# Performance work log

Hardware: AMD Instinct MI355X
Metric: run time of the kernel (lower is better)

Reference implementation:

```python
import jax, jax.numpy as jnp
import numpy as np

N = 50000          # nodes (spots/cells)
E = 1000000        # edges, avg degree 20
IN_DIM, HID, OUT = 256, 128, 64
R = 2              # num_relations
NEG_SLOPE = 0.2    # PyG RGATConv default


def setup_inputs() -> dict:
    key = jax.random.key(0)
    ks = jax.random.split(key, 12)
    features = jax.random.normal(ks[0], (N, IN_DIM), jnp.float32)
    edge_index = jax.random.randint(ks[1], (2, E), 0, N)
    edge_type = jax.random.randint(ks[2], (E,), 0, R)
    s_in, s_hid, s_out = 1.0 / np.sqrt(IN_DIM), 1.0 / np.sqrt(HID), 1.0 / np.sqrt(OUT)
    # RGATConv layer 1 (heads=1, dim=1): relation weights + shared q,k
    W1 = jax.random.normal(ks[3], (R, IN_DIM, HID), jnp.float32) * s_in
    q1 = jax.random.normal(ks[4], (HID, 1), jnp.float32) * s_hid
    k1 = jax.random.normal(ks[5], (HID, 1), jnp.float32) * s_hid
    # RGATConv layer 2
    W2 = jax.random.normal(ks[6], (R, HID, OUT), jnp.float32) * s_hid
    q2 = jax.random.normal(ks[7], (OUT, 1), jnp.float32) * s_out
    k2 = jax.random.normal(ks[8], (OUT, 1), jnp.float32) * s_out
    # decoder: Linear(OUT->HID) then Linear(HID->IN_DIM), biases default-on
    dec_w1 = jax.random.normal(ks[9], (HID, OUT), jnp.float32) * s_out
    dec_b1 = jnp.zeros((HID,), jnp.float32)
    dec_w2 = jax.random.normal(ks[10], (IN_DIM, HID), jnp.float32) * s_hid
    dec_b2 = jnp.zeros((IN_DIM,), jnp.float32)
    return dict(features=features, edge_index=edge_index, edge_type=edge_type,
                W1=W1, q1=q1, k1=k1, W2=W2, q2=q2, k2=k2,
                dec_w1=dec_w1, dec_b1=dec_b1, dec_w2=dec_w2, dec_b2=dec_b2)


def _segment_softmax(alpha, index, num_segments):
    # softmax over edges grouped by destination node (PyG softmax, +1e-16 denom)
    amax = jax.ops.segment_max(alpha, index, num_segments=num_segments)
    amax = jnp.where(jnp.isfinite(amax), amax, 0.0)  # empty segments -> -inf
    ex = jnp.exp(alpha - amax[index])
    denom = jax.ops.segment_sum(ex, index, num_segments=num_segments)
    return ex / (denom[index] + 1e-16)


def _rgat_layer(x, W, q, k, src, dst, edge_type, num_nodes):
    # per-edge x_e @ W[edge_type[e]] == project all nodes per relation, then gather
    proj = jnp.einsum('ni,rio->rno', x, W)          # (R, N, O)
    out_i = proj[edge_type, dst]                    # (E, O) dest-node projection
    out_j = proj[edge_type, src]                    # (E, O) src-node projection
    alpha = jax.nn.leaky_relu(out_i @ q + out_j @ k, NEG_SLOPE)  # (E, 1)
    alpha = _segment_softmax(alpha, dst, num_nodes)
    out = jax.ops.segment_sum(alpha * out_j, dst, num_segments=num_nodes)  # (N, O)
    return out, alpha


def reference(features, edge_index, edge_type, W1, q1, k1, W2, q2, k2,
              dec_w1, dec_b1, dec_w2, dec_b2):
    src, dst = edge_index[0], edge_index[1]
    n = features.shape[0]
    h1, att1 = _rgat_layer(features, W1, q1, k1, src, dst, edge_type, n)
    h1 = jax.nn.elu(h1)
    h2, att2 = _rgat_layer(h1, W2, q2, k2, src, dst, edge_type, n)
    h2 = jax.nn.elu(h2)
    h3 = (h2 @ dec_w1.T + dec_b1) @ dec_w2.T + dec_b2
    return h2, h3, att1, att2
```

## Files before the change

### kernel.cpp

```cpp
#include <hip/hip_runtime.h>
#include <hip/hip_bf16.h>

static constexpr int N_NODES = 50000;
static constexpr int N_EDGE  = 1000000;
static constexpr int IN_D    = 256;
static constexpr int HID_D   = 128;
static constexpr int OUT_D   = 64;
static constexpr int R_REL   = 2;

typedef __attribute__((ext_vector_type(8))) short short8;
typedef __attribute__((ext_vector_type(8))) unsigned short ushort8;
typedef __attribute__((ext_vector_type(4))) float float4v;

static __device__ __forceinline__ unsigned short f2bf(float v) {
    __hip_bfloat16 h = __float2bfloat16(v);
    return *(unsigned short*)&h;
}
static __device__ __forceinline__ float bf2f(unsigned short u) {
    union { unsigned int i; float f; } c; c.i = ((unsigned int)u) << 16; return c.f;
}
static __device__ __forceinline__ float bflo(unsigned u) {
    union { unsigned i; float f; } c; c.i = u << 16; return c.f;
}
static __device__ __forceinline__ float bfhi(unsigned u) {
    union { unsigned i; float f; } c; c.i = u & 0xFFFF0000u; return c.f;
}
static __device__ __forceinline__ float u2f(unsigned u) {
    union { unsigned i; float f; } c; c.i = u; return c.f;
}
static __device__ __forceinline__ unsigned f2u(float f) {
    union { unsigned i; float f; } c; c.f = f; return c.i;
}
static __device__ __forceinline__ void acc8(float w, uint4 v, float (&a)[8]) {
    a[0] = fmaf(w, bflo(v.x), a[0]); a[1] = fmaf(w, bfhi(v.x), a[1]);
    a[2] = fmaf(w, bflo(v.y), a[2]); a[3] = fmaf(w, bfhi(v.y), a[3]);
    a[4] = fmaf(w, bflo(v.z), a[4]); a[5] = fmaf(w, bfhi(v.z), a[5]);
    a[6] = fmaf(w, bflo(v.w), a[6]); a[7] = fmaf(w, bfhi(v.w), a[7]);
}

__global__ __launch_bounds__(256) void prep_k(
    const float* __restrict__ W1, const float* __restrict__ W2,
    const float* __restrict__ dw1, const float* __restrict__ dw2,
    unsigned short* __restrict__ Wc1t, unsigned short* __restrict__ Wc2t,
    unsigned short* __restrict__ dw1h, unsigned short* __restrict__ dw1l,
    unsigned short* __restrict__ dw2h, unsigned short* __restrict__ dw2l)
{
    int idx = blockIdx.x * 256 + threadIdx.x;
    if (idx < R_REL * HID_D * IN_D) {
        const int n = idx / IN_D, kk = idx % IN_D;
        const int r = n / HID_D, o = n % HID_D;
        Wc1t[(long)n * IN_D + kk] = f2bf(W1[((long)r * IN_D + kk) * HID_D + o]);
        return;
    }
    idx -= R_REL * HID_D * IN_D;
    if (idx < R_REL * OUT_D * HID_D) {
        const int n = idx / HID_D, kk = idx % HID_D;
        const int r = n / OUT_D, o = n % OUT_D;
        Wc2t[(long)n * HID_D + kk] = f2bf(W2[((long)r * HID_D + kk) * OUT_D + o]);
        return;
    }
    idx -= R_REL * OUT_D * HID_D;
    if (idx < HID_D * OUT_D) {
        const float v = dw1[idx];
        const unsigned short hi = f2bf(v);
        dw1h[idx] = hi; dw1l[idx] = f2bf(v - bf2f(hi));
        return;
    }
    idx -= HID_D * OUT_D;
    if (idx < IN_D * HID_D) {
        const float v = dw2[idx];
        const unsigned short hi = f2bf(v);
        dw2h[idx] = hi; dw2l[idx] = f2bf(v - bf2f(hi));
    }
}

template<int TM, bool CVT>
__global__ __launch_bounds__(256) void gemm_bf16_k(
    const unsigned short* __restrict__ A, const float* __restrict__ Af,
    const unsigned short* __restrict__ Bt,
    unsigned short* __restrict__ Cb, int M, int K, int Nn)
{
    constexpr int BM = TM * 32;
    constexpr int LDK = 40;
    __shared__ __align__(16) unsigned short As[BM * LDK];
    __shared__ __align__(16) unsigned short Bs[128 * LDK];

    const int tid = threadIdx.x;
    const int wave = tid >> 6, lane = tid & 63;
    const int wm = (wave >> 1) * (TM * 16);
    const int wn = (wave & 1) * 64;
    const int bm = blockIdx.y * BM;
    const int bn = blockIdx.x * 128;
    const int l15 = lane & 15, quad = lane >> 4;

    float4v acc[TM][4];
#pragma unroll
    for (int i = 0; i < TM; ++i)
#pragma unroll
        for (int j = 0; j < 4; ++j) acc[i][j] = (float4v){0.f, 0.f, 0.f, 0.f};

    for (int k0 = 0; k0 < K; k0 += 32) {
        for (int c = tid; c < BM * 4; c += 256) {
            const int r = c >> 2, ch = c & 3;
            const int gr = min(bm + r, M - 1);
            if constexpr (CVT) {
                const float4 f0 = *(const float4*)&Af[(long)gr * K + k0 + ch * 8];
                const float4 f1 = *(const float4*)&Af[(long)gr * K + k0 + ch * 8 + 4];
                uint4 o;
                o.x = (unsigned)f2bf(f0.x) | ((unsigned)f2bf(f0.y) << 16);
                o.y = (unsigned)f2bf(f0.z) | ((unsigned)f2bf(f0.w) << 16);
                o.z = (unsigned)f2bf(f1.x) | ((unsigned)f2bf(f1.y) << 16);
                o.w = (unsigned)f2bf(f1.z) | ((unsigned)f2bf(f1.w) << 16);
                *(uint4*)&As[r * LDK + ch * 8] = o;
            } else {
                *(uint4*)&As[r * LDK + ch * 8] =
                    *(const uint4*)&A[(long)gr * K + k0 + ch * 8];
            }
        }
        for (int c = tid; c < 128 * 4; c += 256) {
            const int r = c >> 2, ch = c & 3;
            *(uint4*)&Bs[r * LDK + ch * 8] =
                *(const uint4*)&Bt[(long)(bn + r) * K + k0 + ch * 8];
        }
        __syncthreads();

        short8 bfrag[4];
#pragma unroll
        for (int nt = 0; nt < 4; ++nt)
            bfrag[nt] = *(const short8*)&Bs[(wn + nt * 16 + l15) * LDK + quad * 8];
#pragma unroll
        for (int mt = 0; mt < TM; ++mt) {
            const short8 afrag = *(const short8*)&As[(wm + mt * 16 + l15) * LDK + quad * 8];
#pragma unroll
            for (int nt = 0; nt < 4; ++nt)
                acc[mt][nt] = __builtin_amdgcn_mfma_f32_16x16x32_bf16(
                    afrag, bfrag[nt], acc[mt][nt], 0, 0, 0);
        }
        __syncthreads();
    }

#pragma unroll
    for (int mt = 0; mt < TM; ++mt)
#pragma unroll
        for (int nt = 0; nt < 4; ++nt) {
            const int n = bn + wn + nt * 16 + l15;
#pragma unroll
            for (int rg = 0; rg < 4; ++rg) {
                const int m = bm + wm + mt * 16 + quad * 4 + rg;
                if (m < M) Cb[(long)m * Nn + n] = f2bf(acc[mt][nt][rg]);
            }
        }
}

template<int TM, bool SPLITOUT>
__global__ __launch_bounds__(256) void dec_gemm_k(
    const unsigned short* __restrict__ Ah, const unsigned short* __restrict__ Al,
    const unsigned short* __restrict__ Bh, const unsigned short* __restrict__ Bl,
    const float* __restrict__ bias, float* __restrict__ Cf,
    unsigned short* __restrict__ Ch, unsigned short* __restrict__ Cl,
    int M, int K, int Nn)
{
    constexpr int BM = TM * 32;
    constexpr int LDK = 40;
    __shared__ __align__(16) unsigned short Ash[BM * LDK];
    __shared__ __align__(16) unsigned short Asl[BM * LDK];
    __shared__ __align__(16) unsigned short Bsh[128 * LDK];
    __shared__ __align__(16) unsigned short Bsl[128 * LDK];

    const int tid = threadIdx.x;
    const int wave = tid >> 6, lane = tid & 63;
    const int wm = (wave >> 1) * (TM * 16);
    const int wn = (wave & 1) * 64;
    const int bm = blockIdx.y * BM;
    const int bn = blockIdx.x * 128;
    const int l15 = lane & 15, quad = lane >> 4;

    float4v acc[TM][4];
#pragma unroll
    for (int i = 0; i < TM; ++i)
#pragma unroll
        for (int j = 0; j < 4; ++j) acc[i][j] = (float4v){0.f, 0.f, 0.f, 0.f};

    for (int k0 = 0; k0 < K; k0 += 32) {
        for (int c = tid; c < BM * 4; c += 256) {
            const int r = c >> 2, ch = c & 3;
            const int gr = min(bm + r, M - 1);
            *(uint4*)&Ash[r * LDK + ch * 8] =
                *(const uint4*)&Ah[(long)gr * K + k0 + ch * 8];
            *(uint4*)&Asl[r * LDK + ch * 8] =
                *(const uint4*)&Al[(long)gr * K + k0 + ch * 8];
        }
        for (int c = tid; c < 128 * 4; c += 256) {
            const int r = c >> 2, ch = c & 3;
            *(uint4*)&Bsh[r * LDK + ch * 8] =
                *(const uint4*)&Bh[(long)(bn + r) * K + k0 + ch * 8];
            *(uint4*)&Bsl[r * LDK + ch * 8] =
                *(const uint4*)&Bl[(long)(bn + r) * K + k0 + ch * 8];
        }
        __syncthreads();

        short8 bh[4], bl[4];
#pragma unroll
        for (int nt = 0; nt < 4; ++nt) {
            bh[nt] = *(const short8*)&Bsh[(wn + nt * 16 + l15) * LDK + quad * 8];
            bl[nt] = *(const short8*)&Bsl[(wn + nt * 16 + l15) * LDK + quad * 8];
        }
#pragma unroll
        for (int mt = 0; mt < TM; ++mt) {
            const short8 ah = *(const short8*)&Ash[(wm + mt * 16 + l15) * LDK + quad * 8];
            const short8 al = *(const short8*)&Asl[(wm + mt * 16 + l15) * LDK + quad * 8];
#pragma unroll
            for (int nt = 0; nt < 4; ++nt) {
                acc[mt][nt] = __builtin_amdgcn_mfma_f32_16x16x32_bf16(ah, bh[nt], acc[mt][nt], 0, 0, 0);
                acc[mt][nt] = __builtin_amdgcn_mfma_f32_16x16x32_bf16(al, bh[nt], acc[mt][nt], 0, 0, 0);
                acc[mt][nt] = __builtin_amdgcn_mfma_f32_16x16x32_bf16(ah, bl[nt], acc[mt][nt], 0, 0, 0);
            }
        }
        __syncthreads();
    }

#pragma unroll
    for (int mt = 0; mt < TM; ++mt)
#pragma unroll
        for (int nt = 0; nt < 4; ++nt) {
            const int n = bn + wn + nt * 16 + l15;
            const float bv = bias[n];
#pragma unroll
            for (int rg = 0; rg < 4; ++rg) {
                const int m = bm + wm + mt * 16 + quad * 4 + rg;
                if (m >= M) continue;
                const float v = acc[mt][nt][rg] + bv;
                if (SPLITOUT) {
                    const unsigned short hi = f2bf(v);
                    Ch[(long)m * Nn + n] = hi;
                    Cl[(long)m * Nn + n] = f2bf(v - bf2f(hi));
                } else {
                    Cf[(long)m * Nn + n] = v;
                }
            }
        }
}

template<int D>
__global__ __launch_bounds__(256) void dotsB_k(
    const unsigned short* __restrict__ projb, const float* __restrict__ q,
    const float* __restrict__ k, float* __restrict__ qd, float* __restrict__ kd,
    int Nn)
{
    const int node = (int)((blockIdx.x * (long)blockDim.x + threadIdx.x) >> 6);
    const int lane = threadIdx.x & 63;
    if (node >= Nn) return;
    const unsigned short* row = projb + (long)node * (2 * D);
    float sq0, sk0, sq1, sk1;
    if (D == 128) {
        const ushort2 a = *(const ushort2*)(row + 2 * lane);
        const ushort2 b = *(const ushort2*)(row + 128 + 2 * lane);
        const float q0 = q[2 * lane], q1 = q[2 * lane + 1];
        const float c0 = k[2 * lane], c1 = k[2 * lane + 1];
        const float a0 = bf2f(a.x), a1 = bf2f(a.y);
        const float b0 = bf2f(b.x), b1 = bf2f(b.y);
        sq0 = fmaf(a0, q0, a1 * q1); sk0 = fmaf(a0, c0, a1 * c1);
        sq1 = fmaf(b0, q0, b1 * q1); sk1 = fmaf(b0, c0, b1 * c1);
    } else {
        const float a0 = bf2f(row[lane]), b0 = bf2f(row[64 + lane]);
        const float q0 = q[lane], c0 = k[lane];
        sq0 = a0 * q0; sk0 = a0 * c0;
        sq1 = b0 * q0; sk1 = b0 * c0;
    }
#pragma unroll
    for (int off = 32; off; off >>= 1) {
        sq0 += __shfl_xor(sq0, off); sk0 += __shfl_xor(sk0, off);
        sq1 += __shfl_xor(sq1, off); sk1 += __shfl_xor(sk1, off);
    }
    if (lane == 0) {
        *(float2*)&qd[2 * node] = make_float2(sq0, sq1);
        kd[node] = sk0; kd[Nn + node] = sk1;
    }
}

__global__ __launch_bounds__(256) void rank_k(
    const int* __restrict__ dstv, int* __restrict__ cnt,
    int* __restrict__ rank, int E)
{
    const int e = blockIdx.x * blockDim.x + threadIdx.x;
    if (e >= E) return;
    rank[e] = atomicAdd(&cnt[dstv[e]], 1);
}

__global__ __launch_bounds__(256) void scan1_k(
    const int* __restrict__ cnt, int* __restrict__ excl_out,
    int* __restrict__ bsum, int n)
{
    __shared__ int s[256];
    const int t = threadIdx.x;
    const int i = blockIdx.x * 256 + t;
    const int v = (i < n) ? cnt[i] : 0;
    s[t] = v;
    __syncthreads();
    for (int off = 1; off < 256; off <<= 1) {
        const int x = (t >= off) ? s[t - off] : 0;
        __syncthreads();
        s[t] += x;
        __syncthreads();
    }
    if (i < n) excl_out[i] = s[t] - v;
    if (t == 255) bsum[blockIdx.x] = s[255];
}

__global__ __launch_bounds__(256) void scan2_k(
    int* __restrict__ bsum, int* __restrict__ bpre, int nb)
{
    __shared__ int s[256];
    const int t = threadIdx.x;
    const int v = (t < nb) ? bsum[t] : 0;
    s[t] = v;
    __syncthreads();
    for (int off = 1; off < 256; off <<= 1) {
        const int x = (t >= off) ? s[t - off] : 0;
        __syncthreads();
        s[t] += x;
        __syncthreads();
    }
    if (t < nb) bpre[t] = s[t] - v;
}

__global__ __launch_bounds__(256) void scan3_k(
    int* __restrict__ excl, const int* __restrict__ bpre,
    int* __restrict__ offs, int n, int total)
{
    const int i = blockIdx.x * 256 + threadIdx.x;
    if (i >= n) return;
    offs[i] = excl[i] + bpre[i >> 8];
    if (i == 0) offs[n] = total;
}

__global__ __launch_bounds__(256) void place_k(
    const int* __restrict__ srcv, const int* __restrict__ dstv,
    const int* __restrict__ et, const int* __restrict__ rank,
    const int* __restrict__ offs, unsigned* __restrict__ recs, int E)
{
    const int e = blockIdx.x * blockDim.x + threadIdx.x;
    if (e >= E) return;
    const int pos = offs[dstv[e]] + rank[e];
    recs[pos] = (unsigned)((et[e] << 16) | srcv[e]);
}

__global__ __launch_bounds__(256) void aggr1_k(
    const int* __restrict__ offs, const unsigned* __restrict__ recs,
    const float* __restrict__ qd, const float* __restrict__ kd,
    const unsigned short* __restrict__ projb,
    float* __restrict__ inv_out, unsigned short* __restrict__ h1b, int Nn)
{
    __shared__ uint2 sh[4][64];
    const int wid = threadIdx.x >> 6;
    const int d = blockIdx.x * 4 + wid;
    const int lane = threadIdx.x & 63;
    if (d >= Nn) return;
    const int beg = offs[d], end = offs[d + 1];
    const float2 qv = *(const float2*)&qd[2 * d];
    const char* pb = (const char*)projb;
    const int quarter = lane >> 4, l15 = lane & 15;
    const unsigned lb = (unsigned)(l15 << 4);
    uint2* shl = sh[wid];

    float exsum = 0.f;
    float a[8] = {0.f, 0.f, 0.f, 0.f, 0.f, 0.f, 0.f, 0.f};

    for (int b = beg; b < end; b += 64) {
        const int i = b + lane;
        float ex = 0.f; unsigned off = 0;
        if (i < end) {
            const unsigned rx = recs[i];
            const int s = (int)(rx & 0xFFFFu), t = (int)(rx >> 16);
            float av = (t ? qv.y : qv.x) + kd[t * Nn + s];
            av = av > 0.f ? av : 0.2f * av;
            ex = __expf(av);
            off = ((unsigned)s << 9) | ((unsigned)t << 8);
        }
        shl[lane] = make_uint2(f2u(ex), off);
        exsum += ex;

        const int cnt = min(64, end - b);
        for (int j = 0; j < cnt; j += 16) {
            const uint2 p0 = shl[j + quarter];
            const uint2 p1 = shl[j + 4 + quarter];
            const uint2 p2 = shl[j + 8 + quarter];
            const uint2 p3 = shl[j + 12 + quarter];
            const uint4 v0 = *(const uint4*)(pb + (p0.y + lb));
            const uint4 v1 = *(const uint4*)(pb + (p1.y + lb));
            const uint4 v2 = *(const uint4*)(pb + (p2.y + lb));
            const uint4 v3 = *(const uint4*)(pb + (p3.y + lb));
            acc8(u2f(p0.x), v0, a);
            acc8(u2f(p1.x), v1, a);
            acc8(u2f(p2.x), v2, a);
            acc8(u2f(p3.x), v3, a);
        }
    }
#pragma unroll
    for (int o = 32; o; o >>= 1) exsum += __shfl_xor(exsum, o);
    const float inv = 1.f / (exsum + 1e-16f);
    if (lane == 0) inv_out[d] = inv;
#pragma unroll
    for (int q = 0; q < 8; ++q) {
        a[q] += __shfl_xor(a[q], 32);
        a[q] += __shfl_xor(a[q], 16);
    }
    if (quarter == 0) {
        ushort8 st;
#pragma unroll
        for (int q = 0; q < 8; ++q) {
            const float e = a[q] * inv;
            st[q] = f2bf(e > 0.f ? e : expm1f(e));
        }
        *(ushort8*)&h1b[(long)d * 128 + (l15 << 3)] = st;
    }
}

__global__ __launch_bounds__(256) void aggr2_k(
    const int* __restrict__ offs, const unsigned* __restrict__ recs,
    const float* __restrict__ qd, const float* __restrict__ kd,
    const unsigned short* __restrict__ projb,
    float* __restrict__ inv_out, float* __restrict__ out,
    unsigned short* __restrict__ h2h, unsigned short* __restrict__ h2l, int Nn)
{
    __shared__ uint2 sh[4][64];
    const int wid = threadIdx.x >> 6;
    const int d = blockIdx.x * 4 + wid;
    const int lane = threadIdx.x & 63;
    if (d >= Nn) return;
    const int beg = offs[d], end = offs[d + 1];
    const float2 qv = *(const float2*)&qd[2 * d];
    const char* pb = (const char*)projb;
    const int eighth = lane >> 3, l7 = lane & 7;
    const unsigned lb = (unsigned)(l7 << 4);
    uint2* shl = sh[wid];

    float exsum = 0.f;
    float a[8] = {0.f, 0.f, 0.f, 0.f, 0.f, 0.f, 0.f, 0.f};

    for (int b = beg; b < end; b += 64) {
        const int i = b + lane;
        float ex = 0.f; unsigned off = 0;
        if (i < end) {
            const unsigned rx = recs[i];
            const int s = (int)(rx & 0xFFFFu), t = (int)(rx >> 16);
            float av = (t ? qv.y : qv.x) + kd[t * Nn + s];
            av = av > 0.f ? av : 0.2f * av;
            ex = __expf(av);
            off = ((unsigned)s << 8) | ((unsigned)t << 7);
        }
        shl[lane] = make_uint2(f2u(ex), off);
        exsum += ex;

        const int cnt = min(64, end - b);
        for (int j = 0; j < cnt; j += 32) {
            const uint2 p0 = shl[j + eighth];
            const uint2 p1 = shl[j + 8 + eighth];
            const uint2 p2 = shl[j + 16 + eighth];
            const uint2 p3 = shl[j + 24 + eighth];
            const uint4 v0 = *(const uint4*)(pb + (p0.y + lb));
            const uint4 v1 = *(const uint4*)(pb + (p1.y + lb));
            const uint4 v2 = *(const uint4*)(pb + (p2.y + lb));
            const uint4 v3 = *(const uint4*)(pb + (p3.y + lb));
            acc8(u2f(p0.x), v0, a);
            acc8(u2f(p1.x), v1, a);
            acc8(u2f(p2.x), v2, a);
            acc8(u2f(p3.x), v3, a);
        }
    }
#pragma unroll
    for (int o = 32; o; o >>= 1) exsum += __shfl_xor(exsum, o);
    const float inv = 1.f / (exsum + 1e-16f);
    if (lane == 0) inv_out[d] = inv;
#pragma unroll
    for (int q = 0; q < 8; ++q) {
        a[q] += __shfl_xor(a[q], 32);
        a[q] += __shfl_xor(a[q], 16);
        a[q] += __shfl_xor(a[q], 8);
    }
    if (eighth == 0) {
        float vv[8];
#pragma unroll
        for (int q = 0; q < 8; ++q) {
            const float e = a[q] * inv;
            vv[q] = e > 0.f ? e : expm1f(e);
        }
        float4 f0; f0.x = vv[0]; f0.y = vv[1]; f0.z = vv[2]; f0.w = vv[3];
        float4 f1; f1.x = vv[4]; f1.y = vv[5]; f1.z = vv[6]; f1.w = vv[7];
        *(float4*)&out[(long)d * 64 + (l7 << 3)] = f0;
        *(float4*)&out[(long)d * 64 + (l7 << 3) + 4] = f1;
        ushort8 hh, hl;
#pragma unroll
        for (int q = 0; q < 8; ++q) {
            const unsigned short hi = f2bf(vv[q]);
            hh[q] = hi; hl[q] = f2bf(vv[q] - bf2f(hi));
        }
        *(ushort8*)&h2h[(long)d * 64 + (l7 << 3)] = hh;
        *(ushort8*)&h2l[(long)d * 64 + (l7 << 3)] = hl;
    }
}

__global__ __launch_bounds__(256) void att_k(
    const int* __restrict__ srcv, const int* __restrict__ dstv,
    const int* __restrict__ et,
    const float* __restrict__ qd1, const float* __restrict__ kd1,
    const float* __restrict__ inv1,
    const float* __restrict__ qd2, const float* __restrict__ kd2,
    const float* __restrict__ inv2,
    float* __restrict__ att1, float* __restrict__ att2, int E, int Nn)
{
    const int e = blockIdx.x * 256 + threadIdx.x;
    if (e >= E) return;
    const int s = srcv[e], d = dstv[e], t = et[e];
    float x1 = qd1[2 * d + t] + kd1[t * Nn + s];
    x1 = x1 > 0.f ? x1 : 0.2f * x1;
    att1[e] = __expf(x1) * inv1[d];
    float x2 = qd2[2 * d + t] + kd2[t * Nn + s];
    x2 = x2 > 0.f ? x2 : 0.2f * x2;
    att2[e] = __expf(x2) * inv2[d];
}

extern "C" void kernel_launch(void* const* d_in, const int* in_sizes, int n_in,
                              void* d_out, int out_size, void* d_ws, size_t ws_size,
                              hipStream_t stream)
{
    const float* features = (const float*)d_in[0];
    const int*   eidx     = (const int*)d_in[1];
    const int*   etype    = (const int*)d_in[2];
    const float* W1       = (const float*)d_in[3];
    const float* q1       = (const float*)d_in[4];
    const float* k1       = (const float*)d_in[5];
    const float* W2       = (const float*)d_in[6];
    const float* q2       = (const float*)d_in[7];
    const float* k2       = (const float*)d_in[8];
    const float* dw1      = (const float*)d_in[9];
    const float* db1      = (const float*)d_in[10];
    const float* dw2      = (const float*)d_in[11];
    const float* db2      = (const float*)d_in[12];

    const int* srcv = eidx;
    const int* dstv = eidx + N_EDGE;

    float* out_h2 = (float*)d_out;
    float* out_h3 = out_h2 + (long)N_NODES * OUT_D;
    float* att1   = out_h3 + (long)N_NODES * IN_D;
    float* att2   = att1 + N_EDGE;

    char* W = (char*)d_ws;
    int* rank = (int*)W;
    unsigned short* projb1 = (unsigned short*)(W);
    unsigned short* projb2 = (unsigned short*)(W);
    unsigned short* hidh   = (unsigned short*)(W);
    unsigned short* hidl   = (unsigned short*)(W + 12800000);
    unsigned short* h1b    = (unsigned short*)(W + 25600000);
    unsigned short* h2h    = (unsigned short*)(W + 25600000 + 12800000);
    unsigned short* h2l    = (unsigned short*)(W + 25600000 + 19200000);
    float* qd1 = (float*)(W + 51200000);
    float* kd1 = qd1 + 2 * N_NODES;
    float* qd2 = kd1 + 2 * N_NODES;
    float* kd2 = qd2 + 2 * N_NODES;
    int* cnt    = (int*)(kd2 + 2 * N_NODES);
    int* offs   = cnt + N_NODES;
    int* bsum   = offs + N_NODES + 1;
    int* bpre   = bsum + 256;
    int* excl   = bpre + 256;
    float* inv1 = (float*)(W + 53500000);
    float* inv2 = inv1 + N_NODES;
    unsigned* recs = (unsigned*)(W + 57300000);
    unsigned short* Wc1t = (unsigned short*)(W + 65300000);
    unsigned short* Wc2t = Wc1t + 65536;
    unsigned short* dw1h = Wc2t + 16384;
    unsigned short* dw1l = dw1h + 8192;
    unsigned short* dw2h = dw1l + 8192;
    unsigned short* dw2l = dw2h + 32768;

    const int NB = (N_NODES + 255) / 256;

    prep_k<<<480, 256, 0, stream>>>(W1, W2, dw1, dw2,
                                    Wc1t, Wc2t, dw1h, dw1l, dw2h, dw2l);

    hipMemsetAsync(cnt, 0, sizeof(int) * N_NODES, stream);
    rank_k<<<(N_EDGE + 255) / 256, 256, 0, stream>>>(dstv, cnt, rank, N_EDGE);
    scan1_k<<<NB, 256, 0, stream>>>(cnt, excl, bsum, N_NODES);
    scan2_k<<<1, 256, 0, stream>>>(bsum, bpre, NB);
    scan3_k<<<NB, 256, 0, stream>>>(excl, bpre, offs, N_NODES, N_EDGE);
    place_k<<<(N_EDGE + 255) / 256, 256, 0, stream>>>(
        srcv, dstv, etype, rank, offs, recs, N_EDGE);

    gemm_bf16_k<4, true><<<dim3(2, (N_NODES + 127) / 128), 256, 0, stream>>>(
        nullptr, features, Wc1t, projb1, N_NODES, IN_D, 2 * HID_D);
    dotsB_k<128><<<(int)(((long)N_NODES * 64 + 255) / 256), 256, 0, stream>>>(
        projb1, q1, k1, qd1, kd1, N_NODES);
    aggr1_k<<<(N_NODES + 3) / 4, 256, 0, stream>>>(
        offs, recs, qd1, kd1, projb1, inv1, h1b, N_NODES);

    gemm_bf16_k<4, false><<<dim3(1, (N_NODES + 127) / 128), 256, 0, stream>>>(
        h1b, nullptr, Wc2t, projb2, N_NODES, HID_D, 2 * OUT_D);
    dotsB_k<64><<<(int)(((long)N_NODES * 64 + 255) / 256), 256, 0, stream>>>(
        projb2, q2, k2, qd2, kd2, N_NODES);
    aggr2_k<<<(N_NODES + 3) / 4, 256, 0, stream>>>(
        offs, recs, qd2, kd2, projb2, inv2, out_h2, h2h, h2l, N_NODES);

    att_k<<<(N_EDGE + 255) / 256, 256, 0, stream>>>(
        srcv, dstv, etype, qd1, kd1, inv1, qd2, kd2, inv2, att1, att2,
        N_EDGE, N_NODES);

    dec_gemm_k<4, true><<<dim3(1, (N_NODES + 127) / 128), 256, 0, stream>>>(
        h2h, h2l, dw1h, dw1l, db1, nullptr, hidh, hidl, N_NODES, OUT_D, HID_D);
    dec_gemm_k<4, false><<<dim3(2, (N_NODES + 127) / 128), 256, 0, stream>>>(
        hidh, hidl, dw2h, dw2l, db2, out_h3, nullptr, nullptr, N_NODES, HID_D, IN_D);
}
```

Before: 420.8 us.

## Register-prefetch next K-tile in GEMMs and halve M-tile to 64 rows

The bf16 GEMM and split-precision decoder GEMM kernels now load the next K-slice from global memory into registers while MFMAs run on the current LDS tile, then commit it to shared memory after the loop. The goal is to hide global load latency behind compute. All four GEMM launches also move from 128-row to 64-row tiles (TM=2), which doubles the block count for better CU occupancy and load balance. In exchange, register pressure rises and B tiles are reloaded more often.

After: 480.6 us. +14.2%, slower.

```diff
diff --git a/kernel.cpp b/kernel.cpp
--- a/kernel.cpp
+++ b/kernel.cpp
@@ -82,6 +82,8 @@
 {
     constexpr int BM = TM * 32;
     constexpr int LDK = 40;
+    constexpr int ACV = BM / 32;
+    constexpr int ABF = BM / 64;
     __shared__ __align__(16) unsigned short As[BM * LDK];
     __shared__ __align__(16) unsigned short Bs[128 * LDK];
 
@@ -93,36 +95,67 @@
     const int bn = blockIdx.x * 128;
     const int l15 = lane & 15, quad = lane >> 4;
 
+    float4 pa[ACV > 0 ? ACV : 1];
+    uint4  qa[ABF > 0 ? ABF : 1];
+    uint4  qb[2];
+
+    auto prefetch = [&](int k0) {
+        if constexpr (CVT) {
+#pragma unroll
+            for (int i = 0; i < ACV; ++i) {
+                const int q = tid + 256 * i, row = q >> 3, c4 = q & 7;
+                const int gr = min(bm + row, M - 1);
+                pa[i] = *(const float4*)&Af[(long)gr * K + k0 + c4 * 4];
+            }
+        } else {
+#pragma unroll
+            for (int i = 0; i < ABF; ++i) {
+                const int q = tid + 256 * i, row = q >> 2, c8 = q & 3;
+                const int gr = min(bm + row, M - 1);
+                qa[i] = *(const uint4*)&A[(long)gr * K + k0 + c8 * 8];
+            }
+        }
+#pragma unroll
+        for (int i = 0; i < 2; ++i) {
+            const int q = tid + 256 * i, row = q >> 2, c8 = q & 3;
+            qb[i] = *(const uint4*)&Bt[(long)(bn + row) * K + k0 + c8 * 8];
+        }
+    };
+    auto commit = [&]() {
+        if constexpr (CVT) {
+#pragma unroll
+            for (int i = 0; i < ACV; ++i) {
+                const int q = tid + 256 * i, row = q >> 3, c4 = q & 7;
+                uint2 o;
+                o.x = (unsigned)f2bf(pa[i].x) | ((unsigned)f2bf(pa[i].y) << 16);
+                o.y = (unsigned)f2bf(pa[i].z) | ((unsigned)f2bf(pa[i].w) << 16);
+                *(uint2*)&As[row * LDK + c4 * 4] = o;
+            }
+        } else {
+#pragma unroll
+            for (int i = 0; i < ABF; ++i) {
+                const int q = tid + 256 * i, row = q >> 2, c8 = q & 3;
+                *(uint4*)&As[row * LDK + c8 * 8] = qa[i];
+            }
+        }
+#pragma unroll
+        for (int i = 0; i < 2; ++i) {
+            const int q = tid + 256 * i, row = q >> 2, c8 = q & 3;
+            *(uint4*)&Bs[row * LDK + c8 * 8] = qb[i];
+        }
+    };
+
     float4v acc[TM][4];
 #pragma unroll
     for (int i = 0; i < TM; ++i)
 #pragma unroll
         for (int j = 0; j < 4; ++j) acc[i][j] = (float4v){0.f, 0.f, 0.f, 0.f};
 
+    prefetch(0);
     for (int k0 = 0; k0 < K; k0 += 32) {
-        for (int c = tid; c < BM * 4; c += 256) {
-            const int r = c >> 2, ch = c & 3;
-            const int gr = min(bm + r, M - 1);
-            if constexpr (CVT) {
-                const float4 f0 = *(const float4*)&Af[(long)gr * K + k0 + ch * 8];
-                const float4 f1 = *(const float4*)&Af[(long)gr * K + k0 + ch * 8 + 4];
-                uint4 o;
-                o.x = (unsigned)f2bf(f0.x) | ((unsigned)f2bf(f0.y) << 16);
-                o.y = (unsigned)f2bf(f0.z) | ((unsigned)f2bf(f0.w) << 16);
-                o.z = (unsigned)f2bf(f1.x) | ((unsigned)f2bf(f1.y) << 16);
-                o.w = (unsigned)f2bf(f1.z) | ((unsigned)f2bf(f1.w) << 16);
-                *(uint4*)&As[r * LDK + ch * 8] = o;
-            } else {
-                *(uint4*)&As[r * LDK + ch * 8] =
-                    *(const uint4*)&A[(long)gr * K + k0 + ch * 8];
-            }
-        }
-        for (int c = tid; c < 128 * 4; c += 256) {
-            const int r = c >> 2, ch = c & 3;
-            *(uint4*)&Bs[r * LDK + ch * 8] =
-                *(const uint4*)&Bt[(long)(bn + r) * K + k0 + ch * 8];
-        }
-        __syncthreads();
+        commit();
+        __syncthreads();
+        if (k0 + 32 < K) prefetch(k0 + 32);
 
         short8 bfrag[4];
 #pragma unroll
@@ -162,6 +195,7 @@
 {
     constexpr int BM = TM * 32;
     constexpr int LDK = 40;
+    constexpr int ABF = BM / 64;
     __shared__ __align__(16) unsigned short Ash[BM * LDK];
     __shared__ __align__(16) unsigned short Asl[BM * LDK];
     __shared__ __align__(16) unsigned short Bsh[128 * LDK];
@@ -175,29 +209,50 @@
     const int bn = blockIdx.x * 128;
     const int l15 = lane & 15, quad = lane >> 4;
 
+    uint4 pah[ABF > 0 ? ABF : 1], pal[ABF > 0 ? ABF : 1];
+    uint4 pbh[2], pbl[2];
+
+    auto prefetch = [&](int k0) {
+#pragma unroll
+        for (int i = 0; i < ABF; ++i) {
+            const int q = tid + 256 * i, row = q >> 2, c8 = q & 3;
+            const int gr = min(bm + row, M - 1);
+            pah[i] = *(const uint4*)&Ah[(long)gr * K + k0 + c8 * 8];
+            pal[i] = *(const uint4*)&Al[(long)gr * K + k0 + c8 * 8];
+        }
+#pragma unroll
+        for (int i = 0; i < 2; ++i) {
+            const int q = tid + 256 * i, row = q >> 2, c8 = q & 3;
+            pbh[i] = *(const uint4*)&Bh[(long)(bn + row) * K + k0 + c8 * 8];
+            pbl[i] = *(const uint4*)&Bl[(long)(bn + row) * K + k0 + c8 * 8];
+        }
+    };
+    auto commit = [&]() {
+#pragma unroll
+        for (int i = 0; i < ABF; ++i) {
+            const int q = tid + 256 * i, row = q >> 2, c8 = q & 3;
+            *(uint4*)&Ash[row * LDK + c8 * 8] = pah[i];
+            *(uint4*)&Asl[row * LDK + c8 * 8] = pal[i];
+        }
+#pragma unroll
+        for (int i = 0; i < 2; ++i) {
+            const int q = tid + 256 * i, row = q >> 2, c8 = q & 3;
+            *(uint4*)&Bsh[row * LDK + c8 * 8] = pbh[i];
+            *(uint4*)&Bsl[row * LDK + c8 * 8] = pbl[i];
+        }
+    };
+
     float4v acc[TM][4];
 #pragma unroll
     for (int i = 0; i < TM; ++i)
 #pragma unroll
         for (int j = 0; j < 4; ++j) acc[i][j] = (float4v){0.f, 0.f, 0.f, 0.f};
 
+    prefetch(0);
     for (int k0 = 0; k0 < K; k0 += 32) {
-        for (int c = tid; c < BM * 4; c += 256) {
-            const int r = c >> 2, ch = c & 3;
-            const int gr = min(bm + r, M - 1);
-            *(uint4*)&Ash[r * LDK + ch * 8] =
-                *(const uint4*)&Ah[(long)gr * K + k0 + ch * 8];
-            *(uint4*)&Asl[r * LDK + ch * 8] =
-                *(const uint4*)&Al[(long)gr * K + k0 + ch * 8];
-        }
-        for (int c = tid; c < 128 * 4; c += 256) {
-            const int r = c >> 2, ch = c & 3;
-            *(uint4*)&Bsh[r * LDK + ch * 8] =
-                *(const uint4*)&Bh[(long)(bn + r) * K + k0 + ch * 8];
-            *(uint4*)&Bsl[r * LDK + ch * 8] =
-                *(const uint4*)&Bl[(long)(bn + r) * K + k0 + ch * 8];
-        }
-        __syncthreads();
+        commit();
+        __syncthreads();
+        if (k0 + 32 < K) prefetch(k0 + 32);
 
         short8 bh[4], bl[4];
 #pragma unroll
@@ -575,6 +630,7 @@
     unsigned short* dw2l = dw2h + 32768;
 
     const int NB = (N_NODES + 255) / 256;
+    const int MB64 = (N_NODES + 63) / 64;
 
     prep_k<<<480, 256, 0, stream>>>(W1, W2, dw1, dw2,
                                     Wc1t, Wc2t, dw1h, dw1l, dw2h, dw2l);
@@ -587,14 +643,14 @@
     place_k<<<(N_EDGE + 255) / 256, 256, 0, stream>>>(
         srcv, dstv, etype, rank, offs, recs, N_EDGE);
 
-    gemm_bf16_k<4, true><<<dim3(2, (N_NODES + 127) / 128), 256, 0, stream>>>(
+    gemm_bf16_k<2, true><<<dim3(2, MB64), 256, 0, stream>>>(
         nullptr, features, Wc1t, projb1, N_NODES, IN_D, 2 * HID_D);
     dotsB_k<128><<<(int)(((long)N_NODES * 64 + 255) / 256), 256, 0, stream>>>(
         projb1, q1, k1, qd1, kd1, N_NODES);
     aggr1_k<<<(N_NODES + 3) / 4, 256, 0, stream>>>(
         offs, recs, qd1, kd1, projb1, inv1, h1b, N_NODES);
 
-    gemm_bf16_k<4, false><<<dim3(1, (N_NODES + 127) / 128), 256, 0, stream>>>(
+    gemm_bf16_k<2, false><<<dim3(1, MB64), 256, 0, stream>>>(
         h1b, nullptr, Wc2t, projb2, N_NODES, HID_D, 2 * OUT_D);
     dotsB_k<64><<<(int)(((long)N_NODES * 64 + 255) / 256), 256, 0, stream>>>(
         projb2, q2, k2, qd2, kd2, N_NODES);
@@ -605,8 +661,8 @@
         srcv, dstv, etype, qd1, kd1, inv1, qd2, kd2, inv2, att1, att2,
         N_EDGE, N_NODES);
 
-    dec_gemm_k<4, true><<<dim3(1, (N_NODES + 127) / 128), 256, 0, stream>>>(
+    dec_gemm_k<2, true><<<dim3(1, MB64), 256, 0, stream>>>(
         h2h, h2l, dw1h, dw1l, db1, nullptr, hidh, hidl, N_NODES, OUT_D, HID_D);
-    dec_gemm_k<4, false><<<dim3(2, (N_NODES + 127) / 128), 256, 0, stream>>>(
+    dec_gemm_k<2, false><<<dim3(2, MB64), 256, 0, stream>>>(
         hidh, hidl, dw2h, dw2l, db2, out_h3, nullptr, nullptr, N_NODES, HID_D, IN_D);
 }
```
